# Kernel tuning notes

Measured on AMD Instinct MI355X. Metric: run time of the kernel, lower is better.

## Reference

```python
import jax, jax.numpy as jnp
import numpy as np

B, S, EMBED, FFN, NQ = 8, 2048, 1024, 4096, 8

def setup_inputs() -> dict:
    key = jax.random.key(0)
    ks = jax.random.split(key, 6)
    return {
        "x": jax.random.normal(ks[0], (B, S, EMBED), dtype=jnp.float32),
        "theta": jax.random.normal(ks[1], (NQ,), dtype=jnp.float32),
        "W1": jax.random.normal(ks[2], (FFN, NQ), dtype=jnp.float32) * (1.0 / np.sqrt(NQ)),
        "b1": jax.random.normal(ks[3], (FFN,), dtype=jnp.float32) * 0.02,
        "W2": jax.random.normal(ks[4], (EMBED, FFN), dtype=jnp.float32) * (1.0 / np.sqrt(FFN)),
        "b2": jax.random.normal(ks[5], (EMBED,), dtype=jnp.float32) * 0.02,
    }

def reference(x, theta, W1, b1, W2, b2):
    # Quantum layer (product circuit, closed form): per qubit i,
    # |0> -RX(x_i)-> -RY(theta_i)->, <PauliZ> = cos(x_i) * cos(theta_i).
    nq = theta.shape[0]
    q = jnp.cos(x[..., :nq]) * jnp.cos(theta)        # [B,S,NQ]
    # dropout is identity in eval mode
    h = jax.nn.relu(jnp.einsum('bsq,fq->bsf', q, W1) + b1)  # [B,S,FFN]
    return jnp.einsum('bsf,ef->bse', h, W2) + b2            # [B,S,EMBED]
```

## Files before the change

kernel.cpp:

```cpp
#include <hip/hip_runtime.h>
#include <cstdint>
#include <cstddef>

#define AS1 __attribute__((address_space(1)))
#define AS3 __attribute__((address_space(3)))

typedef __bf16 bf16x8 __attribute__((ext_vector_type(8)));
typedef float  f32x4  __attribute__((ext_vector_type(4)));

#define MDIM 16384
#define NDIM 1024
#define KDIM 4096
#define NQ   8

__global__ __launch_bounds__(256) void conv_w2_kernel(const float* __restrict__ W2,
                                                      __bf16* __restrict__ W2b) {
    size_t base = ((size_t)blockIdx.x * 256 + threadIdx.x) * 8;
    float4 a = *(const float4*)(W2 + base);
    float4 b = *(const float4*)(W2 + base + 4);
    bf16x8 v;
    v[0] = (__bf16)a.x; v[1] = (__bf16)a.y; v[2] = (__bf16)a.z; v[3] = (__bf16)a.w;
    v[4] = (__bf16)b.x; v[5] = (__bf16)b.y; v[6] = (__bf16)b.z; v[7] = (__bf16)b.w;
    *(bf16x8*)(W2b + base) = v;
}

#define QROWS 32
__global__ __launch_bounds__(256) void qh_kernel(const float* __restrict__ x,
                                                 const float* __restrict__ theta,
                                                 const float* __restrict__ W1,
                                                 const float* __restrict__ b1,
                                                 __bf16* __restrict__ H) {
    __shared__ __align__(16) float qs[QROWS][NQ];
    const int t  = threadIdx.x;
    const int r0 = blockIdx.x * QROWS;

    {
        const int qr = t >> 3, qi = t & 7;
        const float xv = x[(size_t)(r0 + qr) * 1024 + qi];
        qs[qr][qi] = __cosf(xv) * __cosf(theta[qi]);
    }
    __syncthreads();

#pragma unroll
    for (int fc = 0; fc < 2; ++fc) {
        const int f0 = fc * 2048 + t * 8;
        float w[8][8];
#pragma unroll
        for (int fr = 0; fr < 8; ++fr) {
            float4 a = *(const float4*)(W1 + (size_t)(f0 + fr) * NQ);
            float4 b = *(const float4*)(W1 + (size_t)(f0 + fr) * NQ + 4);
            w[fr][0] = a.x; w[fr][1] = a.y; w[fr][2] = a.z; w[fr][3] = a.w;
            w[fr][4] = b.x; w[fr][5] = b.y; w[fr][6] = b.z; w[fr][7] = b.w;
        }
        float bias[8];
        {
            float4 a = *(const float4*)(b1 + f0);
            float4 b = *(const float4*)(b1 + f0 + 4);
            bias[0] = a.x; bias[1] = a.y; bias[2] = a.z; bias[3] = a.w;
            bias[4] = b.x; bias[5] = b.y; bias[6] = b.z; bias[7] = b.w;
        }
#pragma unroll 1
        for (int r = 0; r < QROWS; ++r) {
            const float4 qa = *(const float4*)&qs[r][0];
            const float4 qb = *(const float4*)&qs[r][4];
            float q[8] = { qa.x, qa.y, qa.z, qa.w, qb.x, qb.y, qb.z, qb.w };
            bf16x8 o;
#pragma unroll
            for (int fr = 0; fr < 8; ++fr) {
                float a = bias[fr];
#pragma unroll
                for (int i = 0; i < 8; ++i) a += q[i] * w[fr][i];
                o[fr] = (__bf16)fmaxf(a, 0.f);
            }
            *(bf16x8*)(H + (size_t)(r0 + r) * KDIM + f0) = o;
        }
    }
}

#define BM 256
#define BN 256
#define BK 64
#define SLICE 8192

__device__ __forceinline__ void stage_slice(const __bf16* gsrc, __bf16* ldst) {
    __builtin_amdgcn_global_load_lds((AS1 void*)gsrc, (AS3 void*)ldst, 16, 0, 0);
    __builtin_amdgcn_global_load_lds((AS1 void*)(gsrc + (size_t)128 * KDIM),
                                     (AS3 void*)(ldst + 4096), 16, 0, 0);
}

template<int KS, int MG, bool VM>
__device__ __forceinline__ void phase(const __bf16* bufR, f32x4 (&acc)[8][4],
                                      int axo, int bxo,
                                      const __bf16* gsrc, __bf16* ldst) {
    const __bf16* As = bufR + KS * SLICE;
    const __bf16* Bs = bufR + (2 + KS) * SLICE;
    bf16x8 af[4], bfr[4];
#pragma unroll
    for (int i = 0; i < 4; ++i)
        af[i] = *(const bf16x8*)(As + axo + MG * 2048 + i * 512);
#pragma unroll
    for (int j = 0; j < 4; ++j)
        bfr[j] = *(const bf16x8*)(Bs + bxo + j * 512);
    stage_slice(gsrc, ldst);
    __builtin_amdgcn_s_barrier();
    asm volatile("s_waitcnt lgkmcnt(0)" ::: "memory");
    __builtin_amdgcn_sched_barrier(0);
    __builtin_amdgcn_s_setprio(1);
#pragma unroll
    for (int i = 0; i < 4; ++i)
#pragma unroll
        for (int j = 0; j < 4; ++j)
            acc[MG * 4 + i][j] = __builtin_amdgcn_mfma_f32_16x16x32_bf16(
                af[i], bfr[j], acc[MG * 4 + i][j], 0, 0, 0);
    __builtin_amdgcn_s_setprio(0);
    if constexpr (VM)
        asm volatile("s_waitcnt vmcnt(4)" ::: "memory");
    __builtin_amdgcn_s_barrier();
}

__global__ __launch_bounds__(512, 2) void gemm_bt_kernel(const __bf16* __restrict__ A,
                                                         const __bf16* __restrict__ B,
                                                         const float* __restrict__ bias,
                                                         float* __restrict__ C) {
    __shared__ __align__(16) __bf16 lds[2 * 4 * SLICE];

    const int tid = threadIdx.x;
    const int w   = tid >> 6;
    const int l   = tid & 63;
    const int id  = blockIdx.x;
    const int xcd = id & 7;
    const int s   = id >> 3;
    const int bn  = s & 3;
    const int bm  = xcd * 8 + (s >> 2);

    const int wm = w >> 2;
    const int wn = w & 3;

    const int srow = w * 16 + ((l >> 5) << 3) + (l & 7);
    const int su   = (l >> 3) & 3;
    const __bf16* gA0 = A + (size_t)(bm * BM + srow) * KDIM + su * 8;
    const __bf16* gB0 = B + (size_t)(bn * BN + srow) * KDIM + su * 8;
    const int w512 = w * 512;

    const int ml  = l & 15;
    const int kq  = l >> 4;
    const int lo  = ((ml >> 3) << 8) + ((ml & 7) << 3) + (kq << 6);
    const int axo = wm * 4096 + lo;
    const int bxo = wn * 2048 + lo;

    f32x4 acc[8][4] = {};

    stage_slice(gA0,      lds + 0 * SLICE + w512);
    stage_slice(gB0,      lds + 2 * SLICE + w512);
    stage_slice(gA0 + 32, lds + 1 * SLICE + w512);
    stage_slice(gB0 + 32, lds + 3 * SLICE + w512);
    asm volatile("s_waitcnt vmcnt(4)" ::: "memory");
    __builtin_amdgcn_s_barrier();

#pragma unroll 1
    for (int t = 0; t < KDIM / BK; ++t) {
        const __bf16* bufR = lds + (t & 1) * (4 * SLICE);
        __bf16* bufW = lds + ((t + 1) & 1) * (4 * SLICE);
        const int tn = (t < KDIM / BK - 1) ? (t + 1) * BK : (KDIM / BK - 1) * BK;

        phase<0, 0, false>(bufR, acc, axo, bxo, gA0 + tn,      bufW + 0 * SLICE + w512);
        phase<0, 1, true >(bufR, acc, axo, bxo, gB0 + tn,      bufW + 2 * SLICE + w512);
        phase<1, 0, false>(bufR, acc, axo, bxo, gA0 + tn + 32, bufW + 1 * SLICE + w512);
        phase<1, 1, true >(bufR, acc, axo, bxo, gB0 + tn + 32, bufW + 3 * SLICE + w512);
    }

    const int cm0 = bm * BM + wm * 128;
    const int cn0 = bn * BN + wn * 64;
#pragma unroll
    for (int j = 0; j < 4; ++j) {
        const int col = cn0 + j * 16 + ml;
        const float bv = bias[col];
#pragma unroll
        for (int i = 0; i < 8; ++i) {
            const int row0 = cm0 + i * 16 + kq * 4;
#pragma unroll
            for (int r = 0; r < 4; ++r)
                C[(size_t)(row0 + r) * NDIM + col] = acc[i][j][r] + bv;
        }
    }
}

extern "C" void kernel_launch(void* const* d_in, const int* in_sizes, int n_in,
                              void* d_out, int out_size, void* d_ws, size_t ws_size,
                              hipStream_t stream) {
    const float* x     = (const float*)d_in[0];
    const float* theta = (const float*)d_in[1];
    const float* W1    = (const float*)d_in[2];
    const float* b1    = (const float*)d_in[3];
    const float* W2    = (const float*)d_in[4];
    const float* b2    = (const float*)d_in[5];
    float* out = (float*)d_out;

    __bf16* H   = (__bf16*)d_ws;
    __bf16* W2b = (__bf16*)((char*)d_ws + (size_t)MDIM * KDIM * 2);

    conv_w2_kernel<<<(KDIM * NDIM) / (256 * 8), 256, 0, stream>>>(W2, W2b);
    qh_kernel<<<MDIM / QROWS, 256, 0, stream>>>(x, theta, W1, b1, H);
    gemm_bt_kernel<<<(MDIM / BM) * (NDIM / BN), 512, 0, stream>>>(H, W2b, b2, out);
}
```

Before: 281.8 us.

## Switch GEMM to 32x32x16 MFMA tiles and merge A/B staging phases

Replaces the 16x16x32 bf16 MFMA with 32x32x16 MFMA, so each wave holds a 4x2 grid of 32x32 accumulators instead of 8x4 16x16 tiles. Fragment loads and the epilogue's output row and column mapping are rewritten to match. The four phases per K-tile become two, each staging both A and B slices, which halves the barriers per iteration. Larger MFMA tiles cut LDS fragment reads per FLOP, at the cost of a different LDS access pattern and less interleaving of loads with compute.

```diff
diff --git a/kernel.cpp b/kernel.cpp
--- a/kernel.cpp
+++ b/kernel.cpp
@@ -7,6 +7,7 @@
 
 typedef __bf16 bf16x8 __attribute__((ext_vector_type(8)));
 typedef float  f32x4  __attribute__((ext_vector_type(4)));
+typedef float  f32x16 __attribute__((ext_vector_type(16)));
 
 #define MDIM 16384
 #define NDIM 1024
@@ -88,33 +89,40 @@
                                      (AS3 void*)(ldst + 4096), 16, 0, 0);
 }
 
-template<int KS, int MG, bool VM>
-__device__ __forceinline__ void phase(const __bf16* bufR, f32x4 (&acc)[8][4],
+template<int KS>
+__device__ __forceinline__ void phase(const __bf16* bufR, f32x16 (&acc)[4][2],
                                       int axo, int bxo,
-                                      const __bf16* gsrc, __bf16* ldst) {
+                                      const __bf16* gsrcA, __bf16* ldstA,
+                                      const __bf16* gsrcB, __bf16* ldstB) {
     const __bf16* As = bufR + KS * SLICE;
     const __bf16* Bs = bufR + (2 + KS) * SLICE;
-    bf16x8 af[4], bfr[4];
+    bf16x8 af[4][2], bf[2][2];
 #pragma unroll
     for (int i = 0; i < 4; ++i)
-        af[i] = *(const bf16x8*)(As + axo + MG * 2048 + i * 512);
-#pragma unroll
-    for (int j = 0; j < 4; ++j)
-        bfr[j] = *(const bf16x8*)(Bs + bxo + j * 512);
-    stage_slice(gsrc, ldst);
+#pragma unroll
+        for (int s = 0; s < 2; ++s)
+            af[i][s] = *(const bf16x8*)(As + axo + i * 1024 + s * 128);
+#pragma unroll
+    for (int j = 0; j < 2; ++j)
+#pragma unroll
+        for (int s = 0; s < 2; ++s)
+            bf[j][s] = *(const bf16x8*)(Bs + bxo + j * 1024 + s * 128);
+    stage_slice(gsrcA, ldstA);
+    stage_slice(gsrcB, ldstB);
     __builtin_amdgcn_s_barrier();
     asm volatile("s_waitcnt lgkmcnt(0)" ::: "memory");
     __builtin_amdgcn_sched_barrier(0);
     __builtin_amdgcn_s_setprio(1);
 #pragma unroll
-    for (int i = 0; i < 4; ++i)
-#pragma unroll
-        for (int j = 0; j < 4; ++j)
-            acc[MG * 4 + i][j] = __builtin_amdgcn_mfma_f32_16x16x32_bf16(
-                af[i], bfr[j], acc[MG * 4 + i][j], 0, 0, 0);
+    for (int s = 0; s < 2; ++s)
+#pragma unroll
+        for (int i = 0; i < 4; ++i)
+#pragma unroll
+            for (int j = 0; j < 2; ++j)
+                acc[i][j] = __builtin_amdgcn_mfma_f32_32x32x16_bf16(
+                    af[i][s], bf[j][s], acc[i][j], 0, 0, 0);
     __builtin_amdgcn_s_setprio(0);
-    if constexpr (VM)
-        asm volatile("s_waitcnt vmcnt(4)" ::: "memory");
+    asm volatile("s_waitcnt vmcnt(4)" ::: "memory");
     __builtin_amdgcn_s_barrier();
 }
 
@@ -142,13 +150,13 @@
     const __bf16* gB0 = B + (size_t)(bn * BN + srow) * KDIM + su * 8;
     const int w512 = w * 512;
 
-    const int ml  = l & 15;
-    const int kq  = l >> 4;
-    const int lo  = ((ml >> 3) << 8) + ((ml & 7) << 3) + (kq << 6);
+    const int ml  = l & 31;
+    const int kh  = l >> 5;
+    const int lo  = ((ml >> 3) << 8) + ((ml & 7) << 3) + (kh << 6);
     const int axo = wm * 4096 + lo;
     const int bxo = wn * 2048 + lo;
 
-    f32x4 acc[8][4] = {};
+    f32x16 acc[4][2] = {};
 
     stage_slice(gA0,      lds + 0 * SLICE + w512);
     stage_slice(gB0,      lds + 2 * SLICE + w512);
@@ -163,24 +171,28 @@
         __bf16* bufW = lds + ((t + 1) & 1) * (4 * SLICE);
         const int tn = (t < KDIM / BK - 1) ? (t + 1) * BK : (KDIM / BK - 1) * BK;
 
-        phase<0, 0, false>(bufR, acc, axo, bxo, gA0 + tn,      bufW + 0 * SLICE + w512);
-        phase<0, 1, true >(bufR, acc, axo, bxo, gB0 + tn,      bufW + 2 * SLICE + w512);
-        phase<1, 0, false>(bufR, acc, axo, bxo, gA0 + tn + 32, bufW + 1 * SLICE + w512);
-        phase<1, 1, true >(bufR, acc, axo, bxo, gB0 + tn + 32, bufW + 3 * SLICE + w512);
+        phase<0>(bufR, acc, axo, bxo,
+                 gA0 + tn,      bufW + 0 * SLICE + w512,
+                 gB0 + tn,      bufW + 2 * SLICE + w512);
+        phase<1>(bufR, acc, axo, bxo,
+                 gA0 + tn + 32, bufW + 1 * SLICE + w512,
+                 gB0 + tn + 32, bufW + 3 * SLICE + w512);
     }
 
     const int cm0 = bm * BM + wm * 128;
     const int cn0 = bn * BN + wn * 64;
 #pragma unroll
-    for (int j = 0; j < 4; ++j) {
-        const int col = cn0 + j * 16 + ml;
+    for (int j = 0; j < 2; ++j) {
+        const int col = cn0 + j * 32 + ml;
         const float bv = bias[col];
 #pragma unroll
-        for (int i = 0; i < 8; ++i) {
-            const int row0 = cm0 + i * 16 + kq * 4;
-#pragma unroll
-            for (int r = 0; r < 4; ++r)
-                C[(size_t)(row0 + r) * NDIM + col] = acc[i][j][r] + bv;
+        for (int i = 0; i < 4; ++i) {
+            const int rowbase = cm0 + i * 32 + kh * 4;
+#pragma unroll
+            for (int reg = 0; reg < 16; ++reg) {
+                const int row = rowbase + (reg & 3) + ((reg >> 2) << 3);
+                C[(size_t)row * NDIM + col] = acc[i][j][reg] + bv;
+            }
         }
     }
 }
```

Result: no change. 280.2 us (-0.6%).

## Fuse quantum layer and first FFN matmul into the W2 GEMM mainloop

Applied to the files above, without the earlier changes.

Drops the separate kernel that wrote the 16384x4096 bf16 hidden activation to global memory. The GEMM kernel now computes cos features per row in registers, streams W1 and b1 tiles into LDS, and builds each A-tile of relu(qW1+b1) directly in LDS inside the pipelined K-loop. This removes the large H write and read, at the cost of recomputing H once for each of the four N-tile blocks and adding VALU work and extra barriers inside the MFMA loop.

```diff
diff --git a/kernel.cpp b/kernel.cpp
--- a/kernel.cpp
+++ b/kernel.cpp
@@ -24,59 +24,6 @@
     *(bf16x8*)(W2b + base) = v;
 }
 
-#define QROWS 32
-__global__ __launch_bounds__(256) void qh_kernel(const float* __restrict__ x,
-                                                 const float* __restrict__ theta,
-                                                 const float* __restrict__ W1,
-                                                 const float* __restrict__ b1,
-                                                 __bf16* __restrict__ H) {
-    __shared__ __align__(16) float qs[QROWS][NQ];
-    const int t  = threadIdx.x;
-    const int r0 = blockIdx.x * QROWS;
-
-    {
-        const int qr = t >> 3, qi = t & 7;
-        const float xv = x[(size_t)(r0 + qr) * 1024 + qi];
-        qs[qr][qi] = __cosf(xv) * __cosf(theta[qi]);
-    }
-    __syncthreads();
-
-#pragma unroll
-    for (int fc = 0; fc < 2; ++fc) {
-        const int f0 = fc * 2048 + t * 8;
-        float w[8][8];
-#pragma unroll
-        for (int fr = 0; fr < 8; ++fr) {
-            float4 a = *(const float4*)(W1 + (size_t)(f0 + fr) * NQ);
-            float4 b = *(const float4*)(W1 + (size_t)(f0 + fr) * NQ + 4);
-            w[fr][0] = a.x; w[fr][1] = a.y; w[fr][2] = a.z; w[fr][3] = a.w;
-            w[fr][4] = b.x; w[fr][5] = b.y; w[fr][6] = b.z; w[fr][7] = b.w;
-        }
-        float bias[8];
-        {
-            float4 a = *(const float4*)(b1 + f0);
-            float4 b = *(const float4*)(b1 + f0 + 4);
-            bias[0] = a.x; bias[1] = a.y; bias[2] = a.z; bias[3] = a.w;
-            bias[4] = b.x; bias[5] = b.y; bias[6] = b.z; bias[7] = b.w;
-        }
-#pragma unroll 1
-        for (int r = 0; r < QROWS; ++r) {
-            const float4 qa = *(const float4*)&qs[r][0];
-            const float4 qb = *(const float4*)&qs[r][4];
-            float q[8] = { qa.x, qa.y, qa.z, qa.w, qb.x, qb.y, qb.z, qb.w };
-            bf16x8 o;
-#pragma unroll
-            for (int fr = 0; fr < 8; ++fr) {
-                float a = bias[fr];
-#pragma unroll
-                for (int i = 0; i < 8; ++i) a += q[i] * w[fr][i];
-                o[fr] = (__bf16)fmaxf(a, 0.f);
-            }
-            *(bf16x8*)(H + (size_t)(r0 + r) * KDIM + f0) = o;
-        }
-    }
-}
-
 #define BM 256
 #define BN 256
 #define BK 64
@@ -88,41 +35,16 @@
                                      (AS3 void*)(ldst + 4096), 16, 0, 0);
 }
 
-template<int KS, int MG, bool VM>
-__device__ __forceinline__ void phase(const __bf16* bufR, f32x4 (&acc)[8][4],
-                                      int axo, int bxo,
-                                      const __bf16* gsrc, __bf16* ldst) {
-    const __bf16* As = bufR + KS * SLICE;
-    const __bf16* Bs = bufR + (2 + KS) * SLICE;
-    bf16x8 af[4], bfr[4];
-#pragma unroll
-    for (int i = 0; i < 4; ++i)
-        af[i] = *(const bf16x8*)(As + axo + MG * 2048 + i * 512);
-#pragma unroll
-    for (int j = 0; j < 4; ++j)
-        bfr[j] = *(const bf16x8*)(Bs + bxo + j * 512);
-    stage_slice(gsrc, ldst);
-    __builtin_amdgcn_s_barrier();
-    asm volatile("s_waitcnt lgkmcnt(0)" ::: "memory");
-    __builtin_amdgcn_sched_barrier(0);
-    __builtin_amdgcn_s_setprio(1);
-#pragma unroll
-    for (int i = 0; i < 4; ++i)
-#pragma unroll
-        for (int j = 0; j < 4; ++j)
-            acc[MG * 4 + i][j] = __builtin_amdgcn_mfma_f32_16x16x32_bf16(
-                af[i], bfr[j], acc[MG * 4 + i][j], 0, 0, 0);
-    __builtin_amdgcn_s_setprio(0);
-    if constexpr (VM)
-        asm volatile("s_waitcnt vmcnt(4)" ::: "memory");
-    __builtin_amdgcn_s_barrier();
-}
-
-__global__ __launch_bounds__(512, 2) void gemm_bt_kernel(const __bf16* __restrict__ A,
-                                                         const __bf16* __restrict__ B,
-                                                         const float* __restrict__ bias,
-                                                         float* __restrict__ C) {
+__global__ __launch_bounds__(512, 2) void ffq_fused_kernel(const float* __restrict__ x,
+                                                           const float* __restrict__ theta,
+                                                           const float* __restrict__ W1,
+                                                           const float* __restrict__ b1,
+                                                           const __bf16* __restrict__ B,
+                                                           const float* __restrict__ bias,
+                                                           float* __restrict__ C) {
     __shared__ __align__(16) __bf16 lds[2 * 4 * SLICE];
+    __shared__ __align__(16) float aux[512];
+    __shared__ __align__(16) float auxB[512];
 
     const int tid = threadIdx.x;
     const int w   = tid >> 6;
@@ -138,7 +60,6 @@
 
     const int srow = w * 16 + ((l >> 5) << 3) + (l & 7);
     const int su   = (l >> 3) & 3;
-    const __bf16* gA0 = A + (size_t)(bm * BM + srow) * KDIM + su * 8;
     const __bf16* gB0 = B + (size_t)(bn * BN + srow) * KDIM + su * 8;
     const int w512 = w * 512;
 
@@ -148,25 +69,167 @@
     const int axo = wm * 4096 + lo;
     const int bxo = wn * 2048 + lo;
 
+    float ct[8];
+    {
+        float4 t0 = *(const float4*)theta;
+        float4 t1 = *(const float4*)(theta + 4);
+        ct[0] = __cosf(t0.x); ct[1] = __cosf(t0.y); ct[2] = __cosf(t0.z); ct[3] = __cosf(t0.w);
+        ct[4] = __cosf(t1.x); ct[5] = __cosf(t1.y); ct[6] = __cosf(t1.z); ct[7] = __cosf(t1.w);
+    }
+    float q[4][8];
+#pragma unroll
+    for (int c = 0; c < 4; ++c) {
+        const float* xp = x + (size_t)(bm * BM + c * 64 + l) * 1024;
+        float4 a = *(const float4*)xp;
+        float4 b = *(const float4*)(xp + 4);
+        q[c][0] = __cosf(a.x) * ct[0]; q[c][1] = __cosf(a.y) * ct[1];
+        q[c][2] = __cosf(a.z) * ct[2]; q[c][3] = __cosf(a.w) * ct[3];
+        q[c][4] = __cosf(b.x) * ct[4]; q[c][5] = __cosf(b.y) * ct[5];
+        q[c][6] = __cosf(b.z) * ct[6]; q[c][7] = __cosf(b.w) * ct[7];
+    }
+
+    auto issueW1 = [&](int tf) {
+        __builtin_amdgcn_global_load_lds((AS1 void*)(W1 + ((size_t)tf * 64 + w * 8) * 8 + l),
+                                         (AS3 void*)(aux + w * 64), 4, 0, 0);
+        __builtin_amdgcn_global_load_lds((AS1 void*)(b1 + tf * 64 + w * 8 + (l & 7)),
+                                         (AS3 void*)(auxB + w * 64), 4, 0, 0);
+    };
+    auto computeH = [&](__bf16* Abase) {
+        const float* w1a = aux + w * 64;
+        const float* b1a = auxB + w * 64;
+        float h[4][8];
+#pragma unroll
+        for (int f = 0; f < 8; ++f) {
+            f32x4 wa = *(const f32x4*)(w1a + f * 8);
+            f32x4 wb = *(const f32x4*)(w1a + f * 8 + 4);
+            const float bv = b1a[f];
+#pragma unroll
+            for (int c = 0; c < 4; ++c) {
+                float hv = bv;
+                hv += q[c][0] * wa[0]; hv += q[c][1] * wa[1];
+                hv += q[c][2] * wa[2]; hv += q[c][3] * wa[3];
+                hv += q[c][4] * wb[0]; hv += q[c][5] * wb[1];
+                hv += q[c][6] * wb[2]; hv += q[c][7] * wb[3];
+                h[c][f] = hv;
+            }
+        }
+        __bf16* An = Abase + (w >> 2) * SLICE;
+#pragma unroll
+        for (int c = 0; c < 4; ++c) {
+            const int r = c * 64 + l;
+            bf16x8 o;
+#pragma unroll
+            for (int f = 0; f < 8; ++f) o[f] = (__bf16)fmaxf(h[c][f], 0.f);
+            *(bf16x8*)(An + (((r >> 3) * 32 + (w & 3) * 8 + (r & 7)) << 3)) = o;
+        }
+    };
+
     f32x4 acc[8][4] = {};
 
-    stage_slice(gA0,      lds + 0 * SLICE + w512);
+    issueW1(0);
+    asm volatile("s_waitcnt vmcnt(0)" ::: "memory");
+    computeH(lds);
     stage_slice(gB0,      lds + 2 * SLICE + w512);
-    stage_slice(gA0 + 32, lds + 1 * SLICE + w512);
     stage_slice(gB0 + 32, lds + 3 * SLICE + w512);
-    asm volatile("s_waitcnt vmcnt(4)" ::: "memory");
+    asm volatile("s_waitcnt vmcnt(2)" ::: "memory");
+    asm volatile("s_waitcnt lgkmcnt(0)" ::: "memory");
     __builtin_amdgcn_s_barrier();
 
 #pragma unroll 1
     for (int t = 0; t < KDIM / BK; ++t) {
         const __bf16* bufR = lds + (t & 1) * (4 * SLICE);
         __bf16* bufW = lds + ((t + 1) & 1) * (4 * SLICE);
-        const int tn = (t < KDIM / BK - 1) ? (t + 1) * BK : (KDIM / BK - 1) * BK;
-
-        phase<0, 0, false>(bufR, acc, axo, bxo, gA0 + tn,      bufW + 0 * SLICE + w512);
-        phase<0, 1, true >(bufR, acc, axo, bxo, gB0 + tn,      bufW + 2 * SLICE + w512);
-        phase<1, 0, false>(bufR, acc, axo, bxo, gA0 + tn + 32, bufW + 1 * SLICE + w512);
-        phase<1, 1, true >(bufR, acc, axo, bxo, gB0 + tn + 32, bufW + 3 * SLICE + w512);
+        const int tf  = (t < KDIM / BK - 1) ? t + 1 : KDIM / BK - 1;
+        const int tnB = tf * BK;
+
+        {
+            const __bf16* As = bufR;
+            const __bf16* Bs = bufR + 2 * SLICE;
+            bf16x8 af[4], bfr[4];
+#pragma unroll
+            for (int i = 0; i < 4; ++i) af[i]  = *(const bf16x8*)(As + axo + i * 512);
+#pragma unroll
+            for (int j = 0; j < 4; ++j) bfr[j] = *(const bf16x8*)(Bs + bxo + j * 512);
+            issueW1(tf);
+            stage_slice(gB0 + tnB, bufW + 2 * SLICE + w512);
+            __builtin_amdgcn_s_barrier();
+            asm volatile("s_waitcnt lgkmcnt(0)" ::: "memory");
+            __builtin_amdgcn_sched_barrier(0);
+            __builtin_amdgcn_s_setprio(1);
+#pragma unroll
+            for (int i = 0; i < 4; ++i)
+#pragma unroll
+                for (int j = 0; j < 4; ++j)
+                    acc[i][j] = __builtin_amdgcn_mfma_f32_16x16x32_bf16(af[i], bfr[j], acc[i][j], 0, 0, 0);
+            __builtin_amdgcn_s_setprio(0);
+            __builtin_amdgcn_s_barrier();
+        }
+        {
+            const __bf16* As = bufR;
+            const __bf16* Bs = bufR + 2 * SLICE;
+            bf16x8 af[4], bfr[4];
+#pragma unroll
+            for (int i = 0; i < 4; ++i) af[i]  = *(const bf16x8*)(As + axo + 2048 + i * 512);
+#pragma unroll
+            for (int j = 0; j < 4; ++j) bfr[j] = *(const bf16x8*)(Bs + bxo + j * 512);
+            __builtin_amdgcn_s_barrier();
+            asm volatile("s_waitcnt lgkmcnt(0)" ::: "memory");
+            __builtin_amdgcn_sched_barrier(0);
+            __builtin_amdgcn_s_setprio(1);
+#pragma unroll
+            for (int i = 0; i < 4; ++i)
+#pragma unroll
+                for (int j = 0; j < 4; ++j)
+                    acc[4 + i][j] = __builtin_amdgcn_mfma_f32_16x16x32_bf16(af[i], bfr[j], acc[4 + i][j], 0, 0, 0);
+            __builtin_amdgcn_s_setprio(0);
+            asm volatile("s_waitcnt vmcnt(4)" ::: "memory");
+            __builtin_amdgcn_s_barrier();
+        }
+        {
+            const __bf16* As = bufR + SLICE;
+            const __bf16* Bs = bufR + 3 * SLICE;
+            bf16x8 af[4], bfr[4];
+#pragma unroll
+            for (int i = 0; i < 4; ++i) af[i]  = *(const bf16x8*)(As + axo + i * 512);
+#pragma unroll
+            for (int j = 0; j < 4; ++j) bfr[j] = *(const bf16x8*)(Bs + bxo + j * 512);
+            stage_slice(gB0 + tnB + 32, bufW + 3 * SLICE + w512);
+            __builtin_amdgcn_s_barrier();
+            asm volatile("s_waitcnt lgkmcnt(0)" ::: "memory");
+            __builtin_amdgcn_sched_barrier(0);
+            __builtin_amdgcn_s_setprio(1);
+#pragma unroll
+            for (int i = 0; i < 4; ++i)
+#pragma unroll
+                for (int j = 0; j < 4; ++j)
+                    acc[i][j] = __builtin_amdgcn_mfma_f32_16x16x32_bf16(af[i], bfr[j], acc[i][j], 0, 0, 0);
+            __builtin_amdgcn_s_setprio(0);
+            asm volatile("s_waitcnt vmcnt(4)" ::: "memory");
+            __builtin_amdgcn_s_barrier();
+        }
+        {
+            const __bf16* As = bufR + SLICE;
+            const __bf16* Bs = bufR + 3 * SLICE;
+            bf16x8 af[4], bfr[4];
+#pragma unroll
+            for (int i = 0; i < 4; ++i) af[i]  = *(const bf16x8*)(As + axo + 2048 + i * 512);
+#pragma unroll
+            for (int j = 0; j < 4; ++j) bfr[j] = *(const bf16x8*)(Bs + bxo + j * 512);
+            __builtin_amdgcn_s_barrier();
+            asm volatile("s_waitcnt lgkmcnt(0)" ::: "memory");
+            __builtin_amdgcn_sched_barrier(0);
+            __builtin_amdgcn_s_setprio(1);
+#pragma unroll
+            for (int i = 0; i < 4; ++i)
+#pragma unroll
+                for (int j = 0; j < 4; ++j)
+                    acc[4 + i][j] = __builtin_amdgcn_mfma_f32_16x16x32_bf16(af[i], bfr[j], acc[4 + i][j], 0, 0, 0);
+            __builtin_amdgcn_s_setprio(0);
+            computeH(bufW);
+            asm volatile("s_waitcnt vmcnt(2)" ::: "memory");
+            asm volatile("s_waitcnt lgkmcnt(0)" ::: "memory");
+            __builtin_amdgcn_s_barrier();
+        }
     }
 
     const int cm0 = bm * BM + wm * 128;
@@ -196,10 +259,8 @@
     const float* b2    = (const float*)d_in[5];
     float* out = (float*)d_out;
 
-    __bf16* H   = (__bf16*)d_ws;
-    __bf16* W2b = (__bf16*)((char*)d_ws + (size_t)MDIM * KDIM * 2);
+    __bf16* W2b = (__bf16*)d_ws;
 
     conv_w2_kernel<<<(KDIM * NDIM) / (256 * 8), 256, 0, stream>>>(W2, W2b);
-    qh_kernel<<<MDIM / QROWS, 256, 0, stream>>>(x, theta, W1, b1, H);
-    gemm_bt_kernel<<<(MDIM / BM) * (NDIM / BN), 512, 0, stream>>>(H, W2b, b2, out);
-}
+    ffq_fused_kernel<<<(MDIM / BM) * (NDIM / BN), 512, 0, stream>>>(x, theta, W1, b1, W2b, b2, out);
+}
```

Result: slower. 352.9 us (+25.2%).
